# Kernel optimization log

Hardware: AMD Instinct MI355X
Metric: run time of the kernel (lower is better)

The kernel has to match this reference:

```python
import jax, jax.numpy as jnp
import numpy as np

D_MODEL = 512
N_HEADS = 8
Q_SEQ_LEN = 1024
KV_SEQ_LEN = 1024
N_MODES = 64
D_HEAD = D_MODEL // N_HEADS

# FEDformer frequency_modes (deterministic/lowest branch): lowest n_modes freqs
Q_MODES = np.arange(min(N_MODES, Q_SEQ_LEN // 2))
KV_MODES = np.arange(min(N_MODES, KV_SEQ_LEN // 2))


def setup_inputs() -> dict:
    key = jax.random.key(0)
    kq, kk, kv, kwr, kwi = jax.random.split(key, 5)
    B = 8
    scale = 1.0 / (D_MODEL * D_MODEL)
    return {
        "query": jax.random.normal(kq, (B, N_HEADS, Q_SEQ_LEN, D_HEAD), jnp.float32),
        "key": jax.random.normal(kk, (B, N_HEADS, KV_SEQ_LEN, D_HEAD), jnp.float32),
        "value": jax.random.normal(kv, (B, N_HEADS, KV_SEQ_LEN, D_HEAD), jnp.float32),
        "weights_re": scale * jax.random.uniform(kwr, (N_HEADS, D_HEAD, D_HEAD, len(Q_MODES)), jnp.float32),
        "weights_im": scale * jax.random.uniform(kwi, (N_HEADS, D_HEAD, D_HEAD, len(Q_MODES)), jnp.float32),
    }


def reference(query, key, value, weights_re, weights_im):
    # value is accepted but unused by the original forward (FEA-f variant).
    B, H, L, D = query.shape
    q_modes = jnp.asarray(Q_MODES)
    kv_modes = jnp.asarray(KV_MODES)

    # [B,H,D,L] -> rfft along time -> gather selected frequency modes
    q_fft = jnp.fft.rfft(jnp.swapaxes(query, -2, -1), axis=-1)   # [B,H,D,L//2+1]
    k_fft = jnp.fft.rfft(jnp.swapaxes(key, -2, -1), axis=-1)     # [B,H,D,Lk//2+1]
    q_fft = jnp.take(q_fft, q_modes, axis=-1)                    # [B,H,D,Mq]
    k_fft = jnp.take(k_fft, kv_modes, axis=-1)                   # [B,H,D,Mk]

    # complex attention in frequency domain (no conjugation, as in torch einsum)
    scores_fft = jnp.einsum('bhdq,bhdk->bhqk', q_fft, k_fft)
    attn_fft = jnp.tanh(scores_fft)
    context_fft = jnp.einsum('bhqk,bhdk->bhdq', attn_fft, k_fft)  # [B,H,D,Mq]

    w = (weights_re + 1j * weights_im).astype(jnp.complex64)      # [H,D,D,Mq]
    context_fft = jnp.einsum('bhiq,hijq->bhjq', context_fft, w)   # [B,H,D,Mq]

    # scatter modes back into full rfft spectrum, then irfft
    out_fft = jnp.zeros((B, H, D, L // 2 + 1), jnp.complex64)
    out_fft = out_fft.at[..., q_modes].set(context_fft)
    d_model = H * D
    context = jnp.fft.irfft(out_fft / d_model / d_model, n=L, axis=-1)  # [B,H,D,L]
    return context
```

## Files before the change

kernel.cpp:

```cpp
#include <hip/hip_runtime.h>
#include <hip/hip_bf16.h>
#include <cmath>

#define BATCH 8
#define NH 8
#define BH 64
#define SEQ 1024
#define DH 64
#define NM 64

#define P_PLANE 4096
#define P_FLOATS (2*4*64*2*4096)
#define C1C_OFF  P_FLOATS
#define C2_OFF   (C1C_OFF + 64*64*64*2)

__global__ __launch_bounds__(256) void k_dft(const float* __restrict__ q,
                                             const float* __restrict__ k,
                                             float* __restrict__ P) {
  const int bid = blockIdx.x;
  const int bh = bid & 63;
  const int inp = (bid >> 6) & 1;
  const int tq = bid >> 7;
  const float* x = (inp ? k : q) + (size_t)bh * (SEQ * DH);

  __shared__ float xs[64][64];
  const int tid = threadIdx.x;
  const int mg = tid >> 3;
  const int dg = tid & 7;
  const int m0 = mg * 2, d0 = dg * 8;

  float accr[2][8] = {{0.f}}, acci[2][8] = {{0.f}};

  float stepc[2], steps[2];
#pragma unroll
  for (int mi = 0; mi < 2; ++mi) {
    float ph = (float)(m0 + mi) * (1.0f / 512.0f);
    stepc[mi] = cospif(ph);
    steps[mi] = -sinpif(ph);
  }

  for (int ch = 0; ch < 4; ++ch) {
    const int t0g = tq * 256 + ch * 64;
    const float4* src = reinterpret_cast<const float4*>(x + (size_t)t0g * DH);
    float4* dst = reinterpret_cast<float4*>(&xs[0][0]);
#pragma unroll
    for (int i = 0; i < 4; ++i) dst[tid + i * 256] = src[tid + i * 256];
    __syncthreads();

    float wr[2], wi[2];
#pragma unroll
    for (int mi = 0; mi < 2; ++mi) {
      int p0 = ((m0 + mi) * t0g) & 1023;
      float ph = (float)p0 * (1.0f / 512.0f);
      wr[mi] = cospif(ph);
      wi[mi] = -sinpif(ph);
    }

#pragma unroll 4
    for (int t = 0; t < 64; ++t) {
      float4 a = *reinterpret_cast<const float4*>(&xs[t][d0]);
      float4 b = *reinterpret_cast<const float4*>(&xs[t][d0 + 4]);
      float xv[8] = {a.x, a.y, a.z, a.w, b.x, b.y, b.z, b.w};
#pragma unroll
      for (int mi = 0; mi < 2; ++mi) {
        float cwr = wr[mi], cwi = wi[mi];
#pragma unroll
        for (int di = 0; di < 8; ++di) {
          accr[mi][di] = fmaf(cwr, xv[di], accr[mi][di]);
          acci[mi][di] = fmaf(cwi, xv[di], acci[mi][di]);
        }
        float nr = cwr * stepc[mi] - cwi * steps[mi];
        float ni = cwr * steps[mi] + cwi * stepc[mi];
        wr[mi] = nr; wi[mi] = ni;
      }
    }
    __syncthreads();
  }

  const size_t base = (((size_t)inp * 4 + tq) * 64 + bh) * 2 * P_PLANE;
#pragma unroll
  for (int mi = 0; mi < 2; ++mi) {
    float* pr = P + base + (size_t)(m0 + mi) * 64 + d0;
    float* pi = P + base + P_PLANE + (size_t)(m0 + mi) * 64 + d0;
    *reinterpret_cast<float4*>(pr) =
        make_float4(accr[mi][0], accr[mi][1], accr[mi][2], accr[mi][3]);
    *reinterpret_cast<float4*>(pr + 4) =
        make_float4(accr[mi][4], accr[mi][5], accr[mi][6], accr[mi][7]);
    *reinterpret_cast<float4*>(pi) =
        make_float4(acci[mi][0], acci[mi][1], acci[mi][2], acci[mi][3]);
    *reinterpret_cast<float4*>(pi + 4) =
        make_float4(acci[mi][4], acci[mi][5], acci[mi][6], acci[mi][7]);
  }
}

__device__ __forceinline__ void ctanh_f(float x, float y, float& rr, float& ri) {
  float a = 2.0f * x, b = 2.0f * y;
  if (fabsf(a) > 20.0f) {
    rr = (a > 0.0f) ? 1.0f : -1.0f;
    ri = 0.0f;
  } else {
    float ea = expf(a), ena = expf(-a);
    float sb, cb;
    sincosf(b, &sb, &cb);
    float den = 0.5f * (ea + ena) + cb;
    rr = 0.5f * (ea - ena) / den;
    ri = sb / den;
  }
}

__global__ __launch_bounds__(256) void k_mid_a(const float* __restrict__ P,
                                               float* __restrict__ C1c) {
  __shared__ float Kr[64][68], Ki[64][68];
  __shared__ float Qr[16][68], Qi[16][68];
  __shared__ float Ar[16][68], Ai[16][68];
  __shared__ float C1rs[64][17], C1is[64][17];

  const int tid = threadIdx.x;
  const int bh = blockIdx.x >> 2;
  const int qq = blockIdx.x & 3;

  size_t pq[4], pk[4];
#pragma unroll
  for (int t = 0; t < 4; ++t) {
    pq[t] = (((size_t)(0 * 4 + t) * 64 + bh) * 2) * P_PLANE;
    pk[t] = (((size_t)(1 * 4 + t) * 64 + bh) * 2) * P_PLANE;
  }

  for (int idx = tid; idx < 4096; idx += 256) {
    int kk = idx >> 6, dd = idx & 63;
    float r = 0.f, im = 0.f;
#pragma unroll
    for (int t = 0; t < 4; ++t) {
      r += P[pk[t] + idx];
      im += P[pk[t] + P_PLANE + idx];
    }
    Kr[kk][dd] = r; Ki[kk][dd] = im;
  }
  for (int idx = tid; idx < 1024; idx += 256) {
    int qi2 = idx >> 6, dd = idx & 63;
    int mm = qq * 16 + qi2;
    float r = 0.f, im = 0.f;
#pragma unroll
    for (int t = 0; t < 4; ++t) {
      r += P[pq[t] + mm * 64 + dd];
      im += P[pq[t] + P_PLANE + mm * 64 + dd];
    }
    Qr[qi2][dd] = r; Qi[qi2][dd] = im;
  }
  __syncthreads();

  {
    const int q = tid >> 4, k0 = tid & 15;
    float sr[4] = {0.f}, si[4] = {0.f};
    for (int d = 0; d < 64; d += 4) {
      const float4 qr = *reinterpret_cast<const float4*>(&Qr[q][d]);
      const float4 qi = *reinterpret_cast<const float4*>(&Qi[q][d]);
#pragma unroll
      for (int j = 0; j < 4; ++j) {
        const int kk = k0 + 16 * j;
        const float4 kr = *reinterpret_cast<const float4*>(&Kr[kk][d]);
        const float4 ki = *reinterpret_cast<const float4*>(&Ki[kk][d]);
        float s0 = sr[j], s1 = si[j];
        s0 = fmaf(qr.x, kr.x, s0); s0 = fmaf(-qi.x, ki.x, s0);
        s1 = fmaf(qr.x, ki.x, s1); s1 = fmaf(qi.x, kr.x, s1);
        s0 = fmaf(qr.y, kr.y, s0); s0 = fmaf(-qi.y, ki.y, s0);
        s1 = fmaf(qr.y, ki.y, s1); s1 = fmaf(qi.y, kr.y, s1);
        s0 = fmaf(qr.z, kr.z, s0); s0 = fmaf(-qi.z, ki.z, s0);
        s1 = fmaf(qr.z, ki.z, s1); s1 = fmaf(qi.z, kr.z, s1);
        s0 = fmaf(qr.w, kr.w, s0); s0 = fmaf(-qi.w, ki.w, s0);
        s1 = fmaf(qr.w, ki.w, s1); s1 = fmaf(qi.w, kr.w, s1);
        sr[j] = s0; si[j] = s1;
      }
    }
#pragma unroll
    for (int j = 0; j < 4; ++j) {
      float rr, ri;
      ctanh_f(sr[j], si[j], rr, ri);
      Ar[q][k0 + 16 * j] = rr;
      Ai[q][k0 + 16 * j] = ri;
    }
  }
  __syncthreads();

  {
    const int q = tid >> 4, d0 = (tid & 15) * 4;
    float cr[4] = {0.f}, ci[4] = {0.f};
    for (int kk = 0; kk < 64; ++kk) {
      float ar = Ar[q][kk], ai = Ai[q][kk];
      const float4 kr = *reinterpret_cast<const float4*>(&Kr[kk][d0]);
      const float4 ki = *reinterpret_cast<const float4*>(&Ki[kk][d0]);
      cr[0] = fmaf(ar, kr.x, cr[0]); cr[0] = fmaf(-ai, ki.x, cr[0]);
      ci[0] = fmaf(ar, ki.x, ci[0]); ci[0] = fmaf(ai, kr.x, ci[0]);
      cr[1] = fmaf(ar, kr.y, cr[1]); cr[1] = fmaf(-ai, ki.y, cr[1]);
      ci[1] = fmaf(ar, ki.y, ci[1]); ci[1] = fmaf(ai, kr.y, ci[1]);
      cr[2] = fmaf(ar, kr.z, cr[2]); cr[2] = fmaf(-ai, ki.z, cr[2]);
      ci[2] = fmaf(ar, ki.z, ci[2]); ci[2] = fmaf(ai, kr.z, ci[2]);
      cr[3] = fmaf(ar, kr.w, cr[3]); cr[3] = fmaf(-ai, ki.w, cr[3]);
      ci[3] = fmaf(ar, ki.w, ci[3]); ci[3] = fmaf(ai, kr.w, ci[3]);
    }
#pragma unroll
    for (int j = 0; j < 4; ++j) { C1rs[d0 + j][tid >> 4] = cr[j]; C1is[d0 + j][tid >> 4] = ci[j]; }
  }
  __syncthreads();

  for (int idx = tid; idx < 1024; idx += 256) {
    int i = idx >> 4, ql = idx & 15;
    size_t o = (((size_t)bh * 64 + i) * 64 + qq * 16 + ql) * 2;
    *reinterpret_cast<float2*>(&C1c[o]) = make_float2(C1rs[i][ql], C1is[i][ql]);
  }
}

__global__ __launch_bounds__(64) void k_mid_b(const float* __restrict__ C1c,
                                              const float* __restrict__ wre,
                                              const float* __restrict__ wim,
                                              float* __restrict__ C2) {
  const int bid = blockIdx.x;
  const int j = bid & 63;
  const int h = (bid >> 6) & 7;
  const int bq = bid >> 9;
  const int lane = threadIdx.x;

  const int bh0 = (bq * 2 + 0) * 8 + h;
  const int bh1 = (bq * 2 + 1) * 8 + h;
  const float2* c1a = reinterpret_cast<const float2*>(C1c) + (size_t)bh0 * 4096 + lane;
  const float2* c1b = reinterpret_cast<const float2*>(C1c) + (size_t)bh1 * 4096 + lane;
  const float* wrp = wre + ((size_t)h * 4096 + j) * 64 + lane;
  const float* wip = wim + ((size_t)h * 4096 + j) * 64 + lane;

  float ar0 = 0.f, ai0 = 0.f, ar1 = 0.f, ai1 = 0.f;
#pragma unroll 8
  for (int i = 0; i < 64; ++i) {
    float wr = wrp[(size_t)i * 4096];
    float wi = wip[(size_t)i * 4096];
    float2 ca = c1a[(size_t)i * 64];
    float2 cb = c1b[(size_t)i * 64];
    ar0 = fmaf(ca.x, wr, ar0); ar0 = fmaf(-ca.y, wi, ar0);
    ai0 = fmaf(ca.x, wi, ai0); ai0 = fmaf(ca.y, wr, ai0);
    ar1 = fmaf(cb.x, wr, ar1); ar1 = fmaf(-cb.y, wi, ar1);
    ai1 = fmaf(cb.x, wi, ai1); ai1 = fmaf(cb.y, wr, ai1);
  }
  *reinterpret_cast<float2*>(&C2[(((size_t)bh0 * 64 + j) * 64 + lane) * 2]) = make_float2(ar0, ai0);
  *reinterpret_cast<float2*>(&C2[(((size_t)bh1 * 64 + j) * 64 + lane) * 2]) = make_float2(ar1, ai1);
}

__global__ __launch_bounds__(256) void k_idft(const float* __restrict__ C2,
                                              float* __restrict__ out) {
  __shared__ float Cr[64][68], Ci[64][68];
  const int tid = threadIdx.x;
  const int bh = blockIdx.x >> 3;
  const int tc = blockIdx.x & 7;
  const float s = 1.0f / (512.0f * 512.0f * 1024.0f);

  for (int idx = tid; idx < 4096; idx += 256) {
    int j = idx >> 6, m = idx & 63;
    float f = (m == 0) ? s : 2.0f * s;
    float2 c = *reinterpret_cast<const float2*>(&C2[(((size_t)bh * 64 + j) * 64 + m) * 2]);
    Cr[m][j] = f * c.x;
    Ci[m][j] = f * c.y;
  }
  __syncthreads();

  const int tg = tid & 31, jg = tid >> 5;
  const int t0 = tc * 128 + tg * 4, j0 = jg * 8;

  float sc[4], ss[4], wc[4], wsn[4];
#pragma unroll
  for (int kk = 0; kk < 4; ++kk) {
    float ph = (float)((t0 + kk) & 1023) * (1.0f / 512.0f);
    sc[kk] = cospif(ph);
    ss[kk] = sinpif(ph);
    wc[kk] = 1.0f;
    wsn[kk] = 0.0f;
  }

  float acc[4][8] = {{0.f}};
  for (int m = 0; m < 64; ++m) {
    float4 c0 = *reinterpret_cast<const float4*>(&Cr[m][j0]);
    float4 c1 = *reinterpret_cast<const float4*>(&Cr[m][j0 + 4]);
    float4 e0 = *reinterpret_cast<const float4*>(&Ci[m][j0]);
    float4 e1 = *reinterpret_cast<const float4*>(&Ci[m][j0 + 4]);
    float crv[8] = {c0.x, c0.y, c0.z, c0.w, c1.x, c1.y, c1.z, c1.w};
    float civ[8] = {e0.x, e0.y, e0.z, e0.w, e1.x, e1.y, e1.z, e1.w};
#pragma unroll
    for (int kk = 0; kk < 4; ++kk) {
      float cw = wc[kk], sw = wsn[kk];
#pragma unroll
      for (int jj = 0; jj < 8; ++jj) {
        acc[kk][jj] = fmaf(crv[jj], cw, acc[kk][jj]);
        acc[kk][jj] = fmaf(-civ[jj], sw, acc[kk][jj]);
      }
      float nr = cw * sc[kk] - sw * ss[kk];
      float ni = cw * ss[kk] + sw * sc[kk];
      wc[kk] = nr; wsn[kk] = ni;
    }
  }

#pragma unroll
  for (int jj = 0; jj < 8; ++jj) {
    *reinterpret_cast<float4*>(&out[(size_t)bh * 65536 + (size_t)(j0 + jj) * 1024 + t0]) =
        make_float4(acc[0][jj], acc[1][jj], acc[2][jj], acc[3][jj]);
  }
}

extern "C" void kernel_launch(void* const* d_in, const int* in_sizes, int n_in,
                              void* d_out, int out_size, void* d_ws, size_t ws_size,
                              hipStream_t stream) {
  const float* q   = (const float*)d_in[0];
  const float* k   = (const float*)d_in[1];
  const float* wre = (const float*)d_in[3];
  const float* wim = (const float*)d_in[4];
  float* out = (float*)d_out;
  float* ws  = (float*)d_ws;

  float* P   = ws;
  float* C1c = ws + C1C_OFF;
  float* C2  = ws + C2_OFF;

  k_dft  <<<512,  256, 0, stream>>>(q, k, P);
  k_mid_a<<<256,  256, 0, stream>>>(P, C1c);
  k_mid_b<<<2048,  64, 0, stream>>>(C1c, wre, wim, C2);
  k_idft <<<512,  256, 0, stream>>>(C2, out);
}
```

Baseline: 175.4 us.

## Use precomputed twiddle table in DFT, restructure mid and inverse-DFT kernels

Adds a kernel that precomputes a 1024x64 cos/sin twiddle table. The forward DFT now reads x directly from global memory with one lane per d and scalar-uniform twiddle rows, which drops the shared-memory staging and the rotation recurrence. k_mid_a moves to 512 threads per block. k_mid_b now writes a transposed, prescaled spectrum, so the inverse DFT needs no shared-memory stage and runs one time sample per lane across 2048 blocks. This trades redundant global reads of the table and coefficients, plus one extra launch, for less LDS traffic and synchronisation.

```diff
diff --git a/kernel.cpp b/kernel.cpp
--- a/kernel.cpp
+++ b/kernel.cpp
@@ -13,9 +13,20 @@
 #define P_FLOATS (2*4*64*2*4096)
 #define C1C_OFF  P_FLOATS
 #define C2_OFF   (C1C_OFF + 64*64*64*2)
+#define T_OFF    (C2_OFF + 64*64*64*2)
+
+__global__ __launch_bounds__(256) void k_twid(float* __restrict__ T) {
+  const int idx = blockIdx.x * 256 + threadIdx.x;
+  const int t = idx >> 6, m = idx & 63;
+  const int p = (t * m) & 1023;
+  const float ph = (float)p * (1.0f / 512.0f);
+  T[(size_t)t * 128 + m]      = cospif(ph);
+  T[(size_t)t * 128 + 64 + m] = -sinpif(ph);
+}
 
 __global__ __launch_bounds__(256) void k_dft(const float* __restrict__ q,
                                              const float* __restrict__ k,
+                                             const float* __restrict__ T,
                                              float* __restrict__ P) {
   const int bid = blockIdx.x;
   const int bh = bid & 63;
@@ -23,73 +34,46 @@
   const int tq = bid >> 7;
   const float* x = (inp ? k : q) + (size_t)bh * (SEQ * DH);
 
-  __shared__ float xs[64][64];
   const int tid = threadIdx.x;
-  const int mg = tid >> 3;
-  const int dg = tid & 7;
-  const int m0 = mg * 2, d0 = dg * 8;
-
-  float accr[2][8] = {{0.f}}, acci[2][8] = {{0.f}};
-
-  float stepc[2], steps[2];
-#pragma unroll
-  for (int mi = 0; mi < 2; ++mi) {
-    float ph = (float)(m0 + mi) * (1.0f / 512.0f);
-    stepc[mi] = cospif(ph);
-    steps[mi] = -sinpif(ph);
-  }
-
-  for (int ch = 0; ch < 4; ++ch) {
-    const int t0g = tq * 256 + ch * 64;
-    const float4* src = reinterpret_cast<const float4*>(x + (size_t)t0g * DH);
-    float4* dst = reinterpret_cast<float4*>(&xs[0][0]);
-#pragma unroll
-    for (int i = 0; i < 4; ++i) dst[tid + i * 256] = src[tid + i * 256];
-    __syncthreads();
-
-    float wr[2], wi[2];
-#pragma unroll
-    for (int mi = 0; mi < 2; ++mi) {
-      int p0 = ((m0 + mi) * t0g) & 1023;
-      float ph = (float)p0 * (1.0f / 512.0f);
-      wr[mi] = cospif(ph);
-      wi[mi] = -sinpif(ph);
-    }
+  const int lane = tid & 63;
+  const int wv = __builtin_amdgcn_readfirstlane(tid >> 6);
+  const int m0 = wv * 16;
+
+  float ar[16] = {0.f}, ai[16] = {0.f};
+  const int tbase = tq * 256;
+  const float* xp = x + (size_t)tbase * DH + lane;
+  const float* Tb = T + (size_t)tbase * 128 + m0;
 
 #pragma unroll 4
-    for (int t = 0; t < 64; ++t) {
-      float4 a = *reinterpret_cast<const float4*>(&xs[t][d0]);
-      float4 b = *reinterpret_cast<const float4*>(&xs[t][d0 + 4]);
-      float xv[8] = {a.x, a.y, a.z, a.w, b.x, b.y, b.z, b.w};
-#pragma unroll
-      for (int mi = 0; mi < 2; ++mi) {
-        float cwr = wr[mi], cwi = wi[mi];
-#pragma unroll
-        for (int di = 0; di < 8; ++di) {
-          accr[mi][di] = fmaf(cwr, xv[di], accr[mi][di]);
-          acci[mi][di] = fmaf(cwi, xv[di], acci[mi][di]);
-        }
-        float nr = cwr * stepc[mi] - cwi * steps[mi];
-        float ni = cwr * steps[mi] + cwi * stepc[mi];
-        wr[mi] = nr; wi[mi] = ni;
-      }
-    }
-    __syncthreads();
+  for (int t = 0; t < 256; ++t) {
+    const float xv = xp[(size_t)t * DH];
+    const float4* Tre = reinterpret_cast<const float4*>(Tb + (size_t)t * 128);
+    const float4* Tim = reinterpret_cast<const float4*>(Tb + (size_t)t * 128 + 64);
+    const float4 r0 = Tre[0], r1 = Tre[1], r2 = Tre[2], r3 = Tre[3];
+    const float4 i0 = Tim[0], i1 = Tim[1], i2 = Tim[2], i3 = Tim[3];
+    ar[0]  = fmaf(r0.x, xv, ar[0]);  ai[0]  = fmaf(i0.x, xv, ai[0]);
+    ar[1]  = fmaf(r0.y, xv, ar[1]);  ai[1]  = fmaf(i0.y, xv, ai[1]);
+    ar[2]  = fmaf(r0.z, xv, ar[2]);  ai[2]  = fmaf(i0.z, xv, ai[2]);
+    ar[3]  = fmaf(r0.w, xv, ar[3]);  ai[3]  = fmaf(i0.w, xv, ai[3]);
+    ar[4]  = fmaf(r1.x, xv, ar[4]);  ai[4]  = fmaf(i1.x, xv, ai[4]);
+    ar[5]  = fmaf(r1.y, xv, ar[5]);  ai[5]  = fmaf(i1.y, xv, ai[5]);
+    ar[6]  = fmaf(r1.z, xv, ar[6]);  ai[6]  = fmaf(i1.z, xv, ai[6]);
+    ar[7]  = fmaf(r1.w, xv, ar[7]);  ai[7]  = fmaf(i1.w, xv, ai[7]);
+    ar[8]  = fmaf(r2.x, xv, ar[8]);  ai[8]  = fmaf(i2.x, xv, ai[8]);
+    ar[9]  = fmaf(r2.y, xv, ar[9]);  ai[9]  = fmaf(i2.y, xv, ai[9]);
+    ar[10] = fmaf(r2.z, xv, ar[10]); ai[10] = fmaf(i2.z, xv, ai[10]);
+    ar[11] = fmaf(r2.w, xv, ar[11]); ai[11] = fmaf(i2.w, xv, ai[11]);
+    ar[12] = fmaf(r3.x, xv, ar[12]); ai[12] = fmaf(i3.x, xv, ai[12]);
+    ar[13] = fmaf(r3.y, xv, ar[13]); ai[13] = fmaf(i3.y, xv, ai[13]);
+    ar[14] = fmaf(r3.z, xv, ar[14]); ai[14] = fmaf(i3.z, xv, ai[14]);
+    ar[15] = fmaf(r3.w, xv, ar[15]); ai[15] = fmaf(i3.w, xv, ai[15]);
   }
 
   const size_t base = (((size_t)inp * 4 + tq) * 64 + bh) * 2 * P_PLANE;
 #pragma unroll
-  for (int mi = 0; mi < 2; ++mi) {
-    float* pr = P + base + (size_t)(m0 + mi) * 64 + d0;
-    float* pi = P + base + P_PLANE + (size_t)(m0 + mi) * 64 + d0;
-    *reinterpret_cast<float4*>(pr) =
-        make_float4(accr[mi][0], accr[mi][1], accr[mi][2], accr[mi][3]);
-    *reinterpret_cast<float4*>(pr + 4) =
-        make_float4(accr[mi][4], accr[mi][5], accr[mi][6], accr[mi][7]);
-    *reinterpret_cast<float4*>(pi) =
-        make_float4(acci[mi][0], acci[mi][1], acci[mi][2], acci[mi][3]);
-    *reinterpret_cast<float4*>(pi + 4) =
-        make_float4(acci[mi][4], acci[mi][5], acci[mi][6], acci[mi][7]);
+  for (int mi = 0; mi < 16; ++mi) {
+    P[base + (size_t)(m0 + mi) * 64 + lane]           = ar[mi];
+    P[base + P_PLANE + (size_t)(m0 + mi) * 64 + lane] = ai[mi];
   }
 }
 
@@ -108,7 +92,7 @@
   }
 }
 
-__global__ __launch_bounds__(256) void k_mid_a(const float* __restrict__ P,
+__global__ __launch_bounds__(512) void k_mid_a(const float* __restrict__ P,
                                                float* __restrict__ C1c) {
   __shared__ float Kr[64][68], Ki[64][68];
   __shared__ float Qr[16][68], Qi[16][68];
@@ -126,7 +110,7 @@
     pk[t] = (((size_t)(1 * 4 + t) * 64 + bh) * 2) * P_PLANE;
   }
 
-  for (int idx = tid; idx < 4096; idx += 256) {
+  for (int idx = tid; idx < 4096; idx += 512) {
     int kk = idx >> 6, dd = idx & 63;
     float r = 0.f, im = 0.f;
 #pragma unroll
@@ -136,7 +120,7 @@
     }
     Kr[kk][dd] = r; Ki[kk][dd] = im;
   }
-  for (int idx = tid; idx < 1024; idx += 256) {
+  for (int idx = tid; idx < 1024; idx += 512) {
     int qi2 = idx >> 6, dd = idx & 63;
     int mm = qq * 16 + qi2;
     float r = 0.f, im = 0.f;
@@ -150,14 +134,14 @@
   __syncthreads();
 
   {
-    const int q = tid >> 4, k0 = tid & 15;
-    float sr[4] = {0.f}, si[4] = {0.f};
+    const int q = tid >> 5, k0 = tid & 31;
+    float sr[2] = {0.f}, si[2] = {0.f};
     for (int d = 0; d < 64; d += 4) {
       const float4 qr = *reinterpret_cast<const float4*>(&Qr[q][d]);
       const float4 qi = *reinterpret_cast<const float4*>(&Qi[q][d]);
 #pragma unroll
-      for (int j = 0; j < 4; ++j) {
-        const int kk = k0 + 16 * j;
+      for (int j = 0; j < 2; ++j) {
+        const int kk = k0 + 32 * j;
         const float4 kr = *reinterpret_cast<const float4*>(&Kr[kk][d]);
         const float4 ki = *reinterpret_cast<const float4*>(&Ki[kk][d]);
         float s0 = sr[j], s1 = si[j];
@@ -173,37 +157,33 @@
       }
     }
 #pragma unroll
-    for (int j = 0; j < 4; ++j) {
+    for (int j = 0; j < 2; ++j) {
       float rr, ri;
       ctanh_f(sr[j], si[j], rr, ri);
-      Ar[q][k0 + 16 * j] = rr;
-      Ai[q][k0 + 16 * j] = ri;
+      Ar[q][k0 + 32 * j] = rr;
+      Ai[q][k0 + 32 * j] = ri;
     }
   }
   __syncthreads();
 
   {
-    const int q = tid >> 4, d0 = (tid & 15) * 4;
-    float cr[4] = {0.f}, ci[4] = {0.f};
+    const int q = tid >> 5, d0 = (tid & 31) * 2;
+    float cr[2] = {0.f}, ci[2] = {0.f};
     for (int kk = 0; kk < 64; ++kk) {
-      float ar = Ar[q][kk], ai = Ai[q][kk];
-      const float4 kr = *reinterpret_cast<const float4*>(&Kr[kk][d0]);
-      const float4 ki = *reinterpret_cast<const float4*>(&Ki[kk][d0]);
-      cr[0] = fmaf(ar, kr.x, cr[0]); cr[0] = fmaf(-ai, ki.x, cr[0]);
-      ci[0] = fmaf(ar, ki.x, ci[0]); ci[0] = fmaf(ai, kr.x, ci[0]);
-      cr[1] = fmaf(ar, kr.y, cr[1]); cr[1] = fmaf(-ai, ki.y, cr[1]);
-      ci[1] = fmaf(ar, ki.y, ci[1]); ci[1] = fmaf(ai, kr.y, ci[1]);
-      cr[2] = fmaf(ar, kr.z, cr[2]); cr[2] = fmaf(-ai, ki.z, cr[2]);
-      ci[2] = fmaf(ar, ki.z, ci[2]); ci[2] = fmaf(ai, kr.z, ci[2]);
-      cr[3] = fmaf(ar, kr.w, cr[3]); cr[3] = fmaf(-ai, ki.w, cr[3]);
-      ci[3] = fmaf(ar, ki.w, ci[3]); ci[3] = fmaf(ai, kr.w, ci[3]);
-    }
-#pragma unroll
-    for (int j = 0; j < 4; ++j) { C1rs[d0 + j][tid >> 4] = cr[j]; C1is[d0 + j][tid >> 4] = ci[j]; }
+      float a_r = Ar[q][kk], a_i = Ai[q][kk];
+      const float2 kr = *reinterpret_cast<const float2*>(&Kr[kk][d0]);
+      const float2 ki = *reinterpret_cast<const float2*>(&Ki[kk][d0]);
+      cr[0] = fmaf(a_r, kr.x, cr[0]); cr[0] = fmaf(-a_i, ki.x, cr[0]);
+      ci[0] = fmaf(a_r, ki.x, ci[0]); ci[0] = fmaf(a_i, kr.x, ci[0]);
+      cr[1] = fmaf(a_r, kr.y, cr[1]); cr[1] = fmaf(-a_i, ki.y, cr[1]);
+      ci[1] = fmaf(a_r, ki.y, ci[1]); ci[1] = fmaf(a_i, kr.y, ci[1]);
+    }
+    C1rs[d0][q] = cr[0];     C1is[d0][q] = ci[0];
+    C1rs[d0 + 1][q] = cr[1]; C1is[d0 + 1][q] = ci[1];
   }
   __syncthreads();
 
-  for (int idx = tid; idx < 1024; idx += 256) {
+  for (int idx = tid; idx < 1024; idx += 512) {
     int i = idx >> 4, ql = idx & 15;
     size_t o = (((size_t)bh * 64 + i) * 64 + qq * 16 + ql) * 2;
     *reinterpret_cast<float2*>(&C1c[o]) = make_float2(C1rs[i][ql], C1is[i][ql]);
@@ -213,7 +193,7 @@
 __global__ __launch_bounds__(64) void k_mid_b(const float* __restrict__ C1c,
                                               const float* __restrict__ wre,
                                               const float* __restrict__ wim,
-                                              float* __restrict__ C2) {
+                                              float* __restrict__ C2s) {
   const int bid = blockIdx.x;
   const int j = bid & 63;
   const int h = (bid >> 6) & 7;
@@ -239,66 +219,54 @@
     ar1 = fmaf(cb.x, wr, ar1); ar1 = fmaf(-cb.y, wi, ar1);
     ai1 = fmaf(cb.x, wi, ai1); ai1 = fmaf(cb.y, wr, ai1);
   }
-  *reinterpret_cast<float2*>(&C2[(((size_t)bh0 * 64 + j) * 64 + lane) * 2]) = make_float2(ar0, ai0);
-  *reinterpret_cast<float2*>(&C2[(((size_t)bh1 * 64 + j) * 64 + lane) * 2]) = make_float2(ar1, ai1);
-}
-
-__global__ __launch_bounds__(256) void k_idft(const float* __restrict__ C2,
+  const float s = 1.0f / (512.0f * 512.0f * 1024.0f);
+  const float f = (lane == 0) ? s : 2.0f * s;
+  *reinterpret_cast<float2*>(&C2s[(((size_t)bh0 * 64 + lane) * 64 + j) * 2]) =
+      make_float2(f * ar0, f * ai0);
+  *reinterpret_cast<float2*>(&C2s[(((size_t)bh1 * 64 + lane) * 64 + j) * 2]) =
+      make_float2(f * ar1, f * ai1);
+}
+
+__global__ __launch_bounds__(256) void k_idft(const float* __restrict__ C2s,
                                               float* __restrict__ out) {
-  __shared__ float Cr[64][68], Ci[64][68];
+  const int bid = blockIdx.x;
+  const int jh = bid & 1;
+  const int tc = (bid >> 1) & 15;
+  const int bh = bid >> 5;
+
   const int tid = threadIdx.x;
-  const int bh = blockIdx.x >> 3;
-  const int tc = blockIdx.x & 7;
-  const float s = 1.0f / (512.0f * 512.0f * 1024.0f);
-
-  for (int idx = tid; idx < 4096; idx += 256) {
-    int j = idx >> 6, m = idx & 63;
-    float f = (m == 0) ? s : 2.0f * s;
-    float2 c = *reinterpret_cast<const float2*>(&C2[(((size_t)bh * 64 + j) * 64 + m) * 2]);
-    Cr[m][j] = f * c.x;
-    Ci[m][j] = f * c.y;
-  }
-  __syncthreads();
-
-  const int tg = tid & 31, jg = tid >> 5;
-  const int t0 = tc * 128 + tg * 4, j0 = jg * 8;
-
-  float sc[4], ss[4], wc[4], wsn[4];
-#pragma unroll
-  for (int kk = 0; kk < 4; ++kk) {
-    float ph = (float)((t0 + kk) & 1023) * (1.0f / 512.0f);
-    sc[kk] = cospif(ph);
-    ss[kk] = sinpif(ph);
-    wc[kk] = 1.0f;
-    wsn[kk] = 0.0f;
-  }
-
-  float acc[4][8] = {{0.f}};
+  const int lane = tid & 63;
+  const int wv = __builtin_amdgcn_readfirstlane(tid >> 6);
+  const int j0 = (jh * 4 + wv) * 8;
+  const int t = tc * 64 + lane;
+
+  const float* Cb = C2s + (size_t)bh * 8192 + (size_t)j0 * 2;
+
+  const float ph = (float)t * (1.0f / 512.0f);
+  const float stc = cospif(ph), sts = sinpif(ph);
+  float wr = 1.0f, wi = 0.0f;
+
+  float acc[8] = {0.f};
+#pragma unroll 4
   for (int m = 0; m < 64; ++m) {
-    float4 c0 = *reinterpret_cast<const float4*>(&Cr[m][j0]);
-    float4 c1 = *reinterpret_cast<const float4*>(&Cr[m][j0 + 4]);
-    float4 e0 = *reinterpret_cast<const float4*>(&Ci[m][j0]);
-    float4 e1 = *reinterpret_cast<const float4*>(&Ci[m][j0 + 4]);
-    float crv[8] = {c0.x, c0.y, c0.z, c0.w, c1.x, c1.y, c1.z, c1.w};
-    float civ[8] = {e0.x, e0.y, e0.z, e0.w, e1.x, e1.y, e1.z, e1.w};
-#pragma unroll
-    for (int kk = 0; kk < 4; ++kk) {
-      float cw = wc[kk], sw = wsn[kk];
-#pragma unroll
-      for (int jj = 0; jj < 8; ++jj) {
-        acc[kk][jj] = fmaf(crv[jj], cw, acc[kk][jj]);
-        acc[kk][jj] = fmaf(-civ[jj], sw, acc[kk][jj]);
-      }
-      float nr = cw * sc[kk] - sw * ss[kk];
-      float ni = cw * ss[kk] + sw * sc[kk];
-      wc[kk] = nr; wsn[kk] = ni;
-    }
+    const float4* Cm = reinterpret_cast<const float4*>(Cb + (size_t)m * 128);
+    const float4 b0 = Cm[0], b1 = Cm[1], b2 = Cm[2], b3 = Cm[3];
+    acc[0] = fmaf(b0.x, wr, acc[0]); acc[0] = fmaf(-b0.y, wi, acc[0]);
+    acc[1] = fmaf(b0.z, wr, acc[1]); acc[1] = fmaf(-b0.w, wi, acc[1]);
+    acc[2] = fmaf(b1.x, wr, acc[2]); acc[2] = fmaf(-b1.y, wi, acc[2]);
+    acc[3] = fmaf(b1.z, wr, acc[3]); acc[3] = fmaf(-b1.w, wi, acc[3]);
+    acc[4] = fmaf(b2.x, wr, acc[4]); acc[4] = fmaf(-b2.y, wi, acc[4]);
+    acc[5] = fmaf(b2.z, wr, acc[5]); acc[5] = fmaf(-b2.w, wi, acc[5]);
+    acc[6] = fmaf(b3.x, wr, acc[6]); acc[6] = fmaf(-b3.y, wi, acc[6]);
+    acc[7] = fmaf(b3.z, wr, acc[7]); acc[7] = fmaf(-b3.w, wi, acc[7]);
+    const float nr = wr * stc - wi * sts;
+    const float ni = wr * sts + wi * stc;
+    wr = nr; wi = ni;
   }
 
 #pragma unroll
   for (int jj = 0; jj < 8; ++jj) {
-    *reinterpret_cast<float4*>(&out[(size_t)bh * 65536 + (size_t)(j0 + jj) * 1024 + t0]) =
-        make_float4(acc[0][jj], acc[1][jj], acc[2][jj], acc[3][jj]);
+    out[((size_t)bh * 64 + j0 + jj) * 1024 + t] = acc[jj];
   }
 }
 
@@ -314,10 +282,12 @@
 
   float* P   = ws;
   float* C1c = ws + C1C_OFF;
-  float* C2  = ws + C2_OFF;
-
-  k_dft  <<<512,  256, 0, stream>>>(q, k, P);
-  k_mid_a<<<256,  256, 0, stream>>>(P, C1c);
-  k_mid_b<<<2048,  64, 0, stream>>>(C1c, wre, wim, C2);
-  k_idft <<<512,  256, 0, stream>>>(C2, out);
-}
+  float* C2s = ws + C2_OFF;
+  float* T   = ws + T_OFF;
+
+  k_twid <<<256,  256, 0, stream>>>(T);
+  k_dft  <<<512,  256, 0, stream>>>(q, k, T, P);
+  k_mid_a<<<256,  512, 0, stream>>>(P, C1c);
+  k_mid_b<<<2048,  64, 0, stream>>>(C1c, wre, wim, C2s);
+  k_idft <<<2048, 256, 0, stream>>>(C2s, out);
+}
```

Result: slower. 244.0 us (+39.1%).
